# Optimization experiments

Measured on AMD Instinct MI355X. Metric: run time of the kernel, lower is better.

Reference implementation:

```python
import jax, jax.numpy as jnp
import numpy as np

B, H, S, D = 1, 16, 8192, 64
WINDOW = 1024  # window_size from init; also used as the query block size


def setup_inputs() -> dict:
    key = jax.random.key(0)
    kq, kk, kv = jax.random.split(key, 3)
    Q = jax.random.normal(kq, (B, H, S, D), dtype=jnp.float32)
    K = jax.random.normal(kk, (B, H, S, D), dtype=jnp.float32)
    V = jax.random.normal(kv, (B, H, S, D), dtype=jnp.float32)
    return {"Q": Q, "K": K, "V": V}


def _sliding_window_attn(Q, K, V, window):
    # Banded causal attention: query q attends kv with 0 <= q - kv <= window.
    # Tile queries into blocks of size W=window; each query block i only needs
    # kv positions [i*W - W, i*W + W), i.e. a 2W-wide local slice. This honors
    # the block-sparse structure instead of materializing an SxS score matrix.
    b, h, s, d = Q.shape
    W = window
    nb = s // W  # number of query blocks
    # Pad K,V by W zeros at the front so every block slice is in-bounds.
    Kp = jnp.pad(K, ((0, 0), (0, 0), (W, 0), (0, 0)))
    Vp = jnp.pad(V, ((0, 0), (0, 0), (W, 0), (0, 0)))
    # Local kv indices for each block: block i covers padded positions [i*W, i*W+2W).
    idx = jnp.arange(nb)[:, None] * W + jnp.arange(2 * W)[None, :]  # [nb, 2W]
    Kb = Kp[:, :, idx, :]  # [B,H,nb,2W,D]
    Vb = Vp[:, :, idx, :]  # [B,H,nb,2W,D]
    Qb = Q.reshape(b, h, nb, W, d)  # [B,H,nb,W,D]

    scale = np.float32(1.0 / np.sqrt(d))  # flex_attention default scaling
    scores = jnp.einsum('bhnqd,bhnkd->bhnqk', Qb, Kb) * scale  # [B,H,nb,W,2W]

    # Global positions: q_global = i*W + qi ; kv_global = i*W + kj - W.
    # Mask conds: q>=kv  <=> qi >= kj - W ;  q-kv<=W  <=> qi <= kj ; kv_global>=0.
    qi = jnp.arange(W)[:, None]          # [W,1]
    kj = jnp.arange(2 * W)[None, :]      # [1,2W]
    rel_mask = (qi <= kj) & (qi >= kj - W)                        # [W,2W]
    kv_global = jnp.arange(nb)[:, None, None] * W + kj[None] - W  # [nb,1,2W]
    mask = rel_mask[None] & (kv_global >= 0)                      # [nb,W,2W]

    neg = jnp.finfo(scores.dtype).min
    scores = jnp.where(mask[None, None], scores, neg)
    attn = jax.nn.softmax(scores, axis=-1)
    out = jnp.einsum('bhnqk,bhnkd->bhnqd', attn, Vb)
    return out.reshape(b, h, s, d)


def reference(Q, K, V):
    return _sliding_window_attn(Q, K, V, WINDOW)
```

## Files before the change

### kernel.cpp

```cpp
#include <hip/hip_runtime.h>
#include <stdint.h>

namespace {
constexpr int kH = 16;
constexpr int kS = 8192;
constexpr int kD = 64;
constexpr int kW = 1024;

typedef __attribute__((ext_vector_type(4)))  float float4_t;
typedef __attribute__((ext_vector_type(16))) float f32x16;
typedef __attribute__((ext_vector_type(8)))  short bf16x8;
typedef __attribute__((ext_vector_type(8)))  short short8_t;

__device__ __forceinline__ unsigned short f2bf(float f) {
    union { float fv; uint32_t u; } c; c.fv = f;
    return (unsigned short)((c.u + 0x7fffu + ((c.u >> 16) & 1u)) >> 16);
}

__device__ __forceinline__ float fexp2(float x) {
#if __has_builtin(__builtin_amdgcn_exp2f)
    return __builtin_amdgcn_exp2f(x);
#else
    return exp2f(x);
#endif
}

__device__ __forceinline__ void gload16(const void* g, char* l) {
    __builtin_amdgcn_global_load_lds(
        (const __attribute__((address_space(1))) void*)g,
        (__attribute__((address_space(3))) void*)l, 16, 0, 0);
}

__global__ __launch_bounds__(256)
void prep_k(const float* __restrict__ K, unsigned short* __restrict__ Kb) {
    const int i = (blockIdx.x * 256 + threadIdx.x) * 8;
    float4_t a = *(const float4_t*)(K + i);
    float4_t b = *(const float4_t*)(K + i + 4);
    short8_t o;
    #pragma unroll
    for (int j = 0; j < 4; ++j) { o[j] = (short)f2bf(a[j]); o[j + 4] = (short)f2bf(b[j]); }
    *(short8_t*)(Kb + i) = o;
}

__global__ __launch_bounds__(256)
void prep_v(const float* __restrict__ V, unsigned short* __restrict__ Vt) {
    __shared__ float tile[64][65];
    const int h = blockIdx.y;
    const int s0 = blockIdx.x * 64;
    const int tid = threadIdx.x;
    const size_t hb = (size_t)h * kS * kD;
    #pragma unroll
    for (int it = 0; it < 4; ++it) {
        const int n = tid + it * 256;
        const int s = n >> 4, d0 = (n & 15) * 4;
        float4_t v = *(const float4_t*)(V + hb + (size_t)(s0 + s) * kD + d0);
        tile[s][d0 + 0] = v[0]; tile[s][d0 + 1] = v[1];
        tile[s][d0 + 2] = v[2]; tile[s][d0 + 3] = v[3];
    }
    __syncthreads();
    #pragma unroll
    for (int it = 0; it < 2; ++it) {
        const int n = tid + it * 256;
        const int d = n >> 3, sc = (n & 7) * 8;
        short8_t o;
        #pragma unroll
        for (int j = 0; j < 8; ++j) o[j] = (short)f2bf(tile[sc + j][d]);
        *(short8_t*)(Vt + (size_t)h * kD * kS + (size_t)d * kS + s0 + sc) = o;
    }
}

__global__ __launch_bounds__(256, 4)
void swa_main(const float* __restrict__ Qg, const unsigned short* __restrict__ Kb,
              const unsigned short* __restrict__ Vt, float* __restrict__ Og) {
    __shared__ __align__(16) char lds[2][16384];

    const int lid  = blockIdx.x;
    const int swz  = (lid & 7) * 128 + (lid >> 3);
    const int h    = swz >> 6;
    const int qblk = swz & 63;

    const int tid  = threadIdx.x;
    const int wv   = tid >> 6;
    const int lane = tid & 63;
    const int lq   = lane & 31;
    const int hi   = lane >> 5;

    const int q0b = qblk * 128;
    const int qs  = q0b + wv * 32;
    const int q   = qs + lq;
    const size_t hb  = (size_t)h * kS * kD;
    const size_t hbv = (size_t)h * kD * kS;

    constexpr float qscale = 0.125f * 1.44269504f;
    bf16x8 qf[4];
    {
        const float* qp = Qg + hb + (size_t)q * kD + hi * 8;
        #pragma unroll
        for (int c = 0; c < 4; ++c) {
            float4_t a = *(const float4_t*)(qp + c * 16);
            float4_t b = *(const float4_t*)(qp + c * 16 + 4);
            bf16x8 f;
            #pragma unroll
            for (int j = 0; j < 4; ++j) {
                f[j]     = (short)f2bf(a[j] * qscale);
                f[j + 4] = (short)f2bf(b[j] * qscale);
            }
            qf[c] = f;
        }
    }

    f32x16 acc[2];
    #pragma unroll
    for (int hf = 0; hf < 2; ++hf)
        #pragma unroll
        for (int r = 0; r < 16; ++r) acc[hf][r] = 0.f;
    float l4[4] = {0.f, 0.f, 0.f, 0.f};

    const int kstart = (q0b >= kW) ? q0b - kW : 0;
    const int nt     = (q0b + 128 - kstart) >> 6;

    int srcK[2], srcV[2];
    #pragma unroll
    for (int i = 0; i < 2; ++i) {
        const int n = tid + i * 256;
        const int c = n ^ ((n >> 3) & 7);
        srcK[i] = (c >> 3) * 64 + (c & 7) * 8;
        srcV[i] = (c >> 3) * kS + (c & 7) * 8;
    }
    const unsigned short* KbH = Kb + hb;
    const unsigned short* VtH = Vt + hbv;

    auto stage = [&](int buf, int kb) {
        const unsigned short* Kt = KbH + (size_t)kb * 64;
        const unsigned short* Vq = VtH + kb;
        #pragma unroll
        for (int i = 0; i < 2; ++i) {
            const int db = i * 4096 + wv * 1024;
            gload16(Kt + srcK[i], &lds[buf][db]);
            gload16(Vq + srcV[i], &lds[buf][8192 + db]);
        }
    };

    stage(0, kstart);
    for (int t = 0; t < nt; ++t) {
        const int kb  = kstart + t * 64;
        const int kbn = (t + 1 < nt) ? kb + 64 : kb;
        stage((t + 1) & 1, kbn);
        asm volatile("s_waitcnt vmcnt(4)" ::: "memory");
        __builtin_amdgcn_s_barrier();
        asm volatile("" ::: "memory");

        const char* Kl = lds[t & 1];
        const char* Vl = lds[t & 1] + 8192;

        #pragma unroll
        for (int half = 0; half < 2; ++half) {
            const int kh = kb + half * 32;
            if (kh <= qs && kh >= qs - kW) {
                const int krow = half * 32 + lq;
                const int ksw  = (krow & 7) << 4;
                bf16x8 kf[4];
                #pragma unroll
                for (int c = 0; c < 4; ++c)
                    kf[c] = *(const bf16x8*)(Kl + ((krow * 128 + c * 32 + hi * 16) ^ ksw));

                f32x16 st;
                #pragma unroll
                for (int r = 0; r < 16; ++r) st[r] = 0.f;
                __builtin_amdgcn_s_setprio(1);
                #pragma unroll
                for (int c = 0; c < 4; ++c)
                    st = __builtin_amdgcn_mfma_f32_32x32x16_bf16(kf[c], qf[c], st, 0, 0, 0);
                __builtin_amdgcn_s_setprio(0);

                const int vsw = (lq & 7) << 4;
                bf16x8 vf[4];
                #pragma unroll
                for (int dh = 0; dh < 2; ++dh)
                    #pragma unroll
                    for (int kc = 0; kc < 2; ++kc)
                        vf[dh * 2 + kc] = *(const bf16x8*)(
                            Vl + (((dh * 32 + lq) * 128 + half * 64 + kc * 32 + hi * 16) ^ vsw));

                float p[16];
                const bool interior = (kh <= qs - 32) && (kh >= qs - 992);
                if (interior) {
                    #pragma unroll
                    for (int r = 0; r < 16; ++r) p[r] = fexp2(st[r]);
                } else {
                    #pragma unroll
                    for (int r = 0; r < 16; ++r) {
                        const int ki = kh + (r & 3) + 8 * (r >> 2) + 4 * hi;
                        const bool ok = (ki <= q) && (ki + kW >= q);
                        const float e = fexp2(st[r]);
                        p[r] = ok ? e : 0.f;
                    }
                }
                #pragma unroll
                for (int r = 0; r < 16; ++r) l4[r & 3] += p[r];

                unsigned int wrd[8];
                #pragma unroll
                for (int j = 0; j < 8; ++j)
                    asm("v_cvt_pk_bf16_f32 %0, %1, %2" : "=v"(wrd[j]) : "v"(p[2 * j]), "v"(p[2 * j + 1]));
                asm("v_permlane32_swap_b32 %0, %1" : "+v"(wrd[0]), "+v"(wrd[2]));
                asm("v_permlane32_swap_b32 %0, %1" : "+v"(wrd[1]), "+v"(wrd[3]));
                asm("v_permlane32_swap_b32 %0, %1" : "+v"(wrd[4]), "+v"(wrd[6]));
                asm("v_permlane32_swap_b32 %0, %1" : "+v"(wrd[5]), "+v"(wrd[7]));
                union U { unsigned int u[4]; bf16x8 v; };
                U u0, u1;
                u0.u[0] = wrd[0]; u0.u[1] = wrd[1]; u0.u[2] = wrd[2]; u0.u[3] = wrd[3];
                u1.u[0] = wrd[4]; u1.u[1] = wrd[5]; u1.u[2] = wrd[6]; u1.u[3] = wrd[7];

                __builtin_amdgcn_s_setprio(1);
                acc[0] = __builtin_amdgcn_mfma_f32_32x32x16_bf16(vf[0], u0.v, acc[0], 0, 0, 0);
                acc[1] = __builtin_amdgcn_mfma_f32_32x32x16_bf16(vf[2], u0.v, acc[1], 0, 0, 0);
                acc[0] = __builtin_amdgcn_mfma_f32_32x32x16_bf16(vf[1], u1.v, acc[0], 0, 0, 0);
                acc[1] = __builtin_amdgcn_mfma_f32_32x32x16_bf16(vf[3], u1.v, acc[1], 0, 0, 0);
                __builtin_amdgcn_s_setprio(0);
            }
        }

        asm volatile("" ::: "memory");
        __builtin_amdgcn_s_barrier();
        asm volatile("" ::: "memory");
    }

    float l = (l4[0] + l4[1]) + (l4[2] + l4[3]);
    l += __shfl_xor(l, 32);
    const float rl = 1.f / l;
    float* op = Og + hb + (size_t)q * kD;
    #pragma unroll
    for (int g = 0; g < 4; ++g) {
        float4_t o0, o1;
        #pragma unroll
        for (int j = 0; j < 4; ++j) {
            o0[j] = acc[0][g * 4 + j] * rl;
            o1[j] = acc[1][g * 4 + j] * rl;
        }
        *(float4_t*)(op + g * 8 + hi * 4)      = o0;
        *(float4_t*)(op + 32 + g * 8 + hi * 4) = o1;
    }
}
}

extern "C" void kernel_launch(void* const* d_in, const int* in_sizes, int n_in,
                              void* d_out, int out_size, void* d_ws, size_t ws_size,
                              hipStream_t stream) {
    (void)in_sizes; (void)n_in; (void)out_size; (void)ws_size;
    const float* Q = (const float*)d_in[0];
    const float* K = (const float*)d_in[1];
    const float* V = (const float*)d_in[2];
    float* O = (float*)d_out;
    unsigned short* Kb = (unsigned short*)d_ws;
    unsigned short* Vt = Kb + (size_t)kH * kS * kD;

    prep_k<<<dim3(kH * kS * kD / 2048), dim3(256), 0, stream>>>(K, Kb);
    prep_v<<<dim3(kS / 64, kH), dim3(256), 0, stream>>>(V, Vt);
    swa_main<<<dim3(1024), dim3(256), 0, stream>>>(Q, Kb, Vt, O);
}
```

Measured before the change: 71.86 us.

## Load K fragments directly from global, sum softmax denominators via MFMA, fuse prep kernels

K tiles are no longer staged through LDS. Each wave reads its K fragments straight from global memory into registers, one half-tile ahead, which halves LDS use and the staging traffic. The row sum of the softmax denominator is now computed by an extra MFMA against a ones vector, replacing the per-lane scalar adds and the cross-lane shuffle. The K conversion and V transpose prep kernels are merged into one launch. The trade-offs are that K global loads are now issued per wave without LDS sharing, the vmcnt waits have been moved, and the denominator is accumulated from bf16-rounded probabilities.

Result: slower. 152.2 us (+111.9%).

```diff
diff --git a/kernel.cpp b/kernel.cpp
--- a/kernel.cpp
+++ b/kernel.cpp
@@ -32,23 +32,30 @@
 }
 
 __global__ __launch_bounds__(256)
-void prep_k(const float* __restrict__ K, unsigned short* __restrict__ Kb) {
-    const int i = (blockIdx.x * 256 + threadIdx.x) * 8;
-    float4_t a = *(const float4_t*)(K + i);
-    float4_t b = *(const float4_t*)(K + i + 4);
-    short8_t o;
-    #pragma unroll
-    for (int j = 0; j < 4; ++j) { o[j] = (short)f2bf(a[j]); o[j + 4] = (short)f2bf(b[j]); }
-    *(short8_t*)(Kb + i) = o;
-}
-
-__global__ __launch_bounds__(256)
-void prep_v(const float* __restrict__ V, unsigned short* __restrict__ Vt) {
+void prep_kv(const float* __restrict__ K, const float* __restrict__ V,
+             unsigned short* __restrict__ Kb, unsigned short* __restrict__ Vt) {
     __shared__ float tile[64][65];
-    const int h = blockIdx.y;
+    const int h  = blockIdx.y;
     const int s0 = blockIdx.x * 64;
     const int tid = threadIdx.x;
     const size_t hb = (size_t)h * kS * kD;
+
+    {
+        const size_t base = hb + (size_t)s0 * kD + (size_t)tid * 16;
+        float4_t a = *(const float4_t*)(K + base);
+        float4_t b = *(const float4_t*)(K + base + 4);
+        float4_t c = *(const float4_t*)(K + base + 8);
+        float4_t d = *(const float4_t*)(K + base + 12);
+        short8_t o0, o1;
+        #pragma unroll
+        for (int j = 0; j < 4; ++j) {
+            o0[j] = (short)f2bf(a[j]); o0[j + 4] = (short)f2bf(b[j]);
+            o1[j] = (short)f2bf(c[j]); o1[j + 4] = (short)f2bf(d[j]);
+        }
+        *(short8_t*)(Kb + base)     = o0;
+        *(short8_t*)(Kb + base + 8) = o1;
+    }
+
     #pragma unroll
     for (int it = 0; it < 4; ++it) {
         const int n = tid + it * 256;
@@ -72,7 +79,7 @@
 __global__ __launch_bounds__(256, 4)
 void swa_main(const float* __restrict__ Qg, const unsigned short* __restrict__ Kb,
               const unsigned short* __restrict__ Vt, float* __restrict__ Og) {
-    __shared__ __align__(16) char lds[2][16384];
+    __shared__ __align__(16) char lds[2][8192];
 
     const int lid  = blockIdx.x;
     const int swz  = (lid & 7) * 128 + (lid >> 3);
@@ -109,61 +116,65 @@
         }
     }
 
-    f32x16 acc[2];
-    #pragma unroll
-    for (int hf = 0; hf < 2; ++hf)
-        #pragma unroll
-        for (int r = 0; r < 16; ++r) acc[hf][r] = 0.f;
-    float l4[4] = {0.f, 0.f, 0.f, 0.f};
+    f32x16 acc[2], lsum;
+    #pragma unroll
+    for (int r = 0; r < 16; ++r) { acc[0][r] = 0.f; acc[1][r] = 0.f; lsum[r] = 0.f; }
+
+    bf16x8 ones;
+    #pragma unroll
+    for (int j = 0; j < 8; ++j) ones[j] = (short)0x3F80;
 
     const int kstart = (q0b >= kW) ? q0b - kW : 0;
     const int nt     = (q0b + 128 - kstart) >> 6;
 
-    int srcK[2], srcV[2];
+    int srcV[2];
     #pragma unroll
     for (int i = 0; i < 2; ++i) {
         const int n = tid + i * 256;
         const int c = n ^ ((n >> 3) & 7);
-        srcK[i] = (c >> 3) * 64 + (c & 7) * 8;
         srcV[i] = (c >> 3) * kS + (c & 7) * 8;
     }
     const unsigned short* KbH = Kb + hb;
     const unsigned short* VtH = Vt + hbv;
 
     auto stage = [&](int buf, int kb) {
-        const unsigned short* Kt = KbH + (size_t)kb * 64;
         const unsigned short* Vq = VtH + kb;
         #pragma unroll
-        for (int i = 0; i < 2; ++i) {
-            const int db = i * 4096 + wv * 1024;
-            gload16(Kt + srcK[i], &lds[buf][db]);
-            gload16(Vq + srcV[i], &lds[buf][8192 + db]);
-        }
+        for (int i = 0; i < 2; ++i)
+            gload16(Vq + srcV[i], &lds[buf][i * 4096 + wv * 1024]);
     };
 
+    bf16x8 kf[4];
+    {
+        const unsigned short* kp = KbH + (size_t)(kstart + lq) * kD + hi * 8;
+        #pragma unroll
+        for (int c = 0; c < 4; ++c) kf[c] = *(const bf16x8*)(kp + c * 16);
+    }
     stage(0, kstart);
+    asm volatile("s_waitcnt vmcnt(0)" ::: "memory");
+    __builtin_amdgcn_s_barrier();
+    asm volatile("" ::: "memory");
+
     for (int t = 0; t < nt; ++t) {
         const int kb  = kstart + t * 64;
         const int kbn = (t + 1 < nt) ? kb + 64 : kb;
         stage((t + 1) & 1, kbn);
-        asm volatile("s_waitcnt vmcnt(4)" ::: "memory");
-        __builtin_amdgcn_s_barrier();
-        asm volatile("" ::: "memory");
-
-        const char* Kl = lds[t & 1];
-        const char* Vl = lds[t & 1] + 8192;
+        const char* Vl = lds[t & 1];
 
         #pragma unroll
         for (int half = 0; half < 2; ++half) {
             const int kh = kb + half * 32;
+
+            int khn = kb + 32 * (half + 1);
+            if (khn > kS - 32) khn = kS - 32;
+            bf16x8 kn[4];
+            {
+                const unsigned short* kp = KbH + (size_t)(khn + lq) * kD + hi * 8;
+                #pragma unroll
+                for (int c = 0; c < 4; ++c) kn[c] = *(const bf16x8*)(kp + c * 16);
+            }
+
             if (kh <= qs && kh >= qs - kW) {
-                const int krow = half * 32 + lq;
-                const int ksw  = (krow & 7) << 4;
-                bf16x8 kf[4];
-                #pragma unroll
-                for (int c = 0; c < 4; ++c)
-                    kf[c] = *(const bf16x8*)(Kl + ((krow * 128 + c * 32 + hi * 16) ^ ksw));
-
                 f32x16 st;
                 #pragma unroll
                 for (int r = 0; r < 16; ++r) st[r] = 0.f;
@@ -196,8 +207,6 @@
                         p[r] = ok ? e : 0.f;
                     }
                 }
-                #pragma unroll
-                for (int r = 0; r < 16; ++r) l4[r & 3] += p[r];
 
                 unsigned int wrd[8];
                 #pragma unroll
@@ -215,20 +224,22 @@
                 __builtin_amdgcn_s_setprio(1);
                 acc[0] = __builtin_amdgcn_mfma_f32_32x32x16_bf16(vf[0], u0.v, acc[0], 0, 0, 0);
                 acc[1] = __builtin_amdgcn_mfma_f32_32x32x16_bf16(vf[2], u0.v, acc[1], 0, 0, 0);
+                lsum   = __builtin_amdgcn_mfma_f32_32x32x16_bf16(ones,  u0.v, lsum,   0, 0, 0);
                 acc[0] = __builtin_amdgcn_mfma_f32_32x32x16_bf16(vf[1], u1.v, acc[0], 0, 0, 0);
                 acc[1] = __builtin_amdgcn_mfma_f32_32x32x16_bf16(vf[3], u1.v, acc[1], 0, 0, 0);
+                lsum   = __builtin_amdgcn_mfma_f32_32x32x16_bf16(ones,  u1.v, lsum,   0, 0, 0);
                 __builtin_amdgcn_s_setprio(0);
             }
-        }
-
-        asm volatile("" ::: "memory");
+
+            kf[0] = kn[0]; kf[1] = kn[1]; kf[2] = kn[2]; kf[3] = kn[3];
+        }
+
+        asm volatile("s_waitcnt vmcnt(4)" ::: "memory");
         __builtin_amdgcn_s_barrier();
         asm volatile("" ::: "memory");
     }
 
-    float l = (l4[0] + l4[1]) + (l4[2] + l4[3]);
-    l += __shfl_xor(l, 32);
-    const float rl = 1.f / l;
+    const float rl = 1.f / lsum[0];
     float* op = Og + hb + (size_t)q * kD;
     #pragma unroll
     for (int g = 0; g < 4; ++g) {
@@ -255,7 +266,6 @@
     unsigned short* Kb = (unsigned short*)d_ws;
     unsigned short* Vt = Kb + (size_t)kH * kS * kD;
 
-    prep_k<<<dim3(kH * kS * kD / 2048), dim3(256), 0, stream>>>(K, Kb);
-    prep_v<<<dim3(kS / 64, kH), dim3(256), 0, stream>>>(V, Vt);
+    prep_kv<<<dim3(kS / 64, kH), dim3(256), 0, stream>>>(K, V, Kb, Vt);
     swa_main<<<dim3(1024), dim3(256), 0, stream>>>(Q, Kb, Vt, O);
 }
```
